# Optimization experiments

Hardware: AMD Instinct MI355X
Metric: run time of the kernel (lower is better)

Reference implementation:

```python
import jax, jax.numpy as jnp
import numpy as np

DN = ('NCHW', 'OIHW', 'NCHW')

def bn(x, g, b, m, v, eps=1e-5):
    # inference-mode BatchNorm2d over channel dim of NCHW
    s = g * jax.lax.rsqrt(v + eps)
    return x * s[:, None, None] + (b - m * s)[:, None, None]

def conv2d(x, w, pad):
    return jax.lax.conv_general_dilated(x, w, (1, 1), pad, dimension_numbers=DN)

def mamba(x, in_w, cw, cb, xp_w, dt_w, dt_b, A_log, Dp, out_w):
    # x: [B, L, d_model]
    B, L, dm = x.shape
    di = cw.shape[0]           # d_inner
    N = A_log.shape[1]         # d_state
    R = dt_w.shape[1]          # dt_rank
    K = cw.shape[2]            # d_conv
    xz = x @ in_w.T            # [B, L, 2*di]
    xi, z = xz[..., :di], xz[..., di:]
    # causal depthwise conv1d along L
    xc = jnp.transpose(xi, (0, 2, 1))  # [B, di, L]
    xc = jax.lax.conv_general_dilated(xc, cw, (1,), [(K - 1, 0)],
                                      dimension_numbers=('NCH', 'OIH', 'NCH'),
                                      feature_group_count=di)
    xc = jax.nn.silu(xc + cb[None, :, None])
    xc = jnp.transpose(xc, (0, 2, 1))  # [B, L, di]
    dbl = xc @ xp_w.T                  # [B, L, R+2N]
    dt, Bs, Cs = dbl[..., :R], dbl[..., R:R + N], dbl[..., R + N:]
    dt = jax.nn.softplus(dt @ dt_w.T + dt_b)        # [B, L, di]
    A = -jnp.exp(A_log)                              # [di, N]
    dA = jnp.exp(dt[..., None] * A)                  # [B, L, di, N]
    dBx = dt[..., None] * Bs[:, :, None, :] * xc[..., None]  # [B, L, di, N]

    def step(h, inp):
        a, bx, c = inp                               # [B,di,N],[B,di,N],[B,N]
        h = a * h + bx
        return h, jnp.einsum('bdn,bn->bd', h, c)

    h0 = jnp.zeros((B, di, N), x.dtype)
    _, ys = jax.lax.scan(step, h0, (jnp.transpose(dA, (1, 0, 2, 3)),
                                    jnp.transpose(dBx, (1, 0, 2, 3)),
                                    jnp.transpose(Cs, (1, 0, 2))))
    y = jnp.transpose(ys, (1, 0, 2)) + xc * Dp       # skip via D
    y = y * jax.nn.silu(z)                           # gate
    return y @ out_w.T                               # [B, L, dm]

def fwd(x, w1, g1, b1, m1, v1, w2, g2, b2, m2, v2,
        in_w, cw, cb, xp_w, dt_w, dt_b, A_log, Dp, out_w,
        w3, g3, b3, m3, v3, w4, g4, b4, m4, v4):
    x = jax.nn.gelu(bn(conv2d(x, w1, [(1, 1), (1, 1)]), g1, b1, m1, v1), approximate=False)
    x = jax.nn.silu(bn(conv2d(x, w2, [(0, 0), (0, 0)]), g2, b2, m2, v2))
    Bsz, Dc, H, W = x.shape
    t = jnp.transpose(x, (0, 2, 3, 1)).reshape(Bsz, H * W, Dc)
    t = mamba(t, in_w, cw, cb, xp_w, dt_w, dt_b, A_log, Dp, out_w)
    x = jnp.transpose(t.reshape(Bsz, H, W, Dc), (0, 3, 1, 2))
    x = jax.nn.silu(bn(conv2d(x, w3, [(0, 0), (0, 0)]), g3, b3, m3, v3))
    x = jax.nn.gelu(bn(conv2d(x, w4, [(1, 1), (1, 1)]), g4, b4, m4, v4), approximate=False)
    return x

def setup_inputs() -> dict:
    INC, D, OUTC = 96, 192, 192
    DI, N, R, K = 2 * D, 16, 12, 4   # d_inner, d_state, dt_rank, d_conv
    B, H, W = 8, 32, 32
    ks = jax.random.split(jax.random.key(0), 32)
    rn = lambda i, sh, s=0.05: s * jax.random.normal(ks[i], sh, dtype=jnp.float32)
    def bnp(i, c):
        k1, k2, k3, k4 = jax.random.split(ks[i], 4)
        return (1.0 + 0.1 * jax.random.normal(k1, (c,), dtype=jnp.float32),
                0.1 * jax.random.normal(k2, (c,), dtype=jnp.float32),
                0.1 * jax.random.normal(k3, (c,), dtype=jnp.float32),
                jax.random.uniform(k4, (c,), jnp.float32, 0.5, 1.5))
    g1, b1, m1, v1 = bnp(2, INC)
    g2, b2, m2, v2 = bnp(4, D)
    g3, b3, m3, v3 = bnp(6, OUTC)
    g4, b4, m4, v4 = bnp(8, OUTC)
    A_log = jnp.log(jnp.broadcast_to(jnp.arange(1, N + 1, dtype=jnp.float32), (DI, N)))
    return {
        'x': jax.random.normal(ks[0], (B, INC, H, W), dtype=jnp.float32),
        'w1': rn(1, (INC, INC, 3, 3)), 'g1': g1, 'b1': b1, 'm1': m1, 'v1': v1,
        'w2': rn(3, (D, INC, 1, 1)), 'g2': g2, 'b2': b2, 'm2': m2, 'v2': v2,
        'in_w': rn(10, (2 * DI, D), 0.02),
        'cw': rn(11, (DI, 1, K), 0.2),
        'cb': rn(12, (DI,), 0.02),
        'xp_w': rn(13, (R + 2 * N, DI), 0.05),
        'dt_w': rn(14, (DI, R), 0.1),
        'dt_b': rn(15, (DI,), 0.1) - 4.0,
        'A_log': A_log,
        'Dp': jnp.ones((DI,), dtype=jnp.float32),
        'out_w': rn(16, (D, DI), 0.05),
        'w3': rn(5, (OUTC, D, 1, 1)), 'g3': g3, 'b3': b3, 'm3': m3, 'v3': v3,
        'w4': rn(7, (OUTC, OUTC, 3, 3), 0.03), 'g4': g4, 'b4': b4, 'm4': m4, 'v4': v4,
    }

def reference(x, w1, g1, b1, m1, v1, w2, g2, b2, m2, v2,
              in_w, cw, cb, xp_w, dt_w, dt_b, A_log, Dp, out_w,
              w3, g3, b3, m3, v3, w4, g4, b4, m4, v4):
    return fwd(x, w1, g1, b1, m1, v1, w2, g2, b2, m2, v2,
               in_w, cw, cb, xp_w, dt_w, dt_b, A_log, Dp, out_w,
               w3, g3, b3, m3, v3, w4, g4, b4, m4, v4)
```

## Files before the change

kernel.cpp:

```cpp
#include <hip/hip_runtime.h>
#include <hip/hip_bf16.h>

using u16 = unsigned short;
using short8 = __attribute__((ext_vector_type(8))) short;
using f32x4  = __attribute__((ext_vector_type(4))) float;

constexpr int DI_ = 384;

constexpr size_t O_XZ   = 0;
constexpr size_t O_XCT  = O_XZ  + (size_t)8192*384;
constexpr size_t O_ZST  = O_XCT + (size_t)384*8192;
constexpr size_t O_DBLT = O_ZST + (size_t)384*8192;
constexpr size_t O_YFT  = O_DBLT+ (size_t)32*8192;
constexpr size_t O_B16  = O_YFT + (size_t)384*8192;
constexpr size_t O_DTT  = O_XZ;
constexpr size_t B_T1  = 0;
constexpr size_t B_T2  = B_T1  + (size_t)8192*96;
constexpr size_t B_XC  = B_T2  + (size_t)8192*192;
constexpr size_t B_XB1 = B_XC  + (size_t)8192*384;
constexpr size_t B_XB4 = B_XB1 + (size_t)8192*96;
constexpr size_t B_WT1 = B_XB4 + (size_t)8192*192;
constexpr size_t B_WT4 = B_WT1 + (size_t)9*96*96;
constexpr size_t B_INW = B_WT4 + (size_t)9*192*192;
constexpr size_t B_W2  = B_INW + (size_t)768*192;
constexpr size_t B_XP  = B_W2  + (size_t)192*96;
constexpr size_t B_WDT = B_XP  + (size_t)32*384;
constexpr size_t B_WOW = B_WDT + (size_t)384*384;

__device__ __forceinline__ u16 f2b(float f) {
    __hip_bfloat16 h = __float2bfloat16(f);
    return *reinterpret_cast<u16*>(&h);
}

struct PrepArgs {
    const float *w1, *w4, *in_w, *w2, *xp_w, *dt_w, *w3, *out_w, *x;
    u16 *wt1, *wt4, *inwb, *w2b, *xpb, *Wdt, *Wow, *Xb1;
};

__global__ __launch_bounds__(256) void prep_k(PrepArgs a) {
    const int job = blockIdx.y;
    const int stride = gridDim.x * 256;
    const int i0 = blockIdx.x * 256 + threadIdx.x;
    switch (job) {
    case 0:
        for (int i = i0; i < 9*96*96; i += stride) {
            int ci = i % 96, co = (i / 96) % 96, t = i / (96*96);
            a.wt1[i] = f2b(a.w1[((size_t)co*96 + ci)*9 + t]);
        } break;
    case 1:
        for (int i = i0; i < 9*192*192; i += stride) {
            int ci = i % 192, co = (i / 192) % 192, t = i / (192*192);
            a.wt4[i] = f2b(a.w4[((size_t)co*192 + ci)*9 + t]);
        } break;
    case 2:
        for (int i = i0; i < 768*192; i += stride) a.inwb[i] = f2b(a.in_w[i]);
        break;
    case 3:
        for (int i = i0; i < 192*96; i += stride) a.w2b[i] = f2b(a.w2[i]);
        break;
    case 4:
        for (int i = i0; i < 32*384; i += stride) {
            int r = i / 384, c = i % 384;
            a.xpb[i] = f2b(a.xp_w[(size_t)(12 + r)*384 + c]);
        } break;
    case 5:
        for (int i = i0; i < 384*384; i += stride) {
            int r = i / 384, c = i % 384;
            float s = 0.f;
            #pragma unroll
            for (int k = 0; k < 12; ++k) s += a.dt_w[r*12 + k] * a.xp_w[(size_t)k*384 + c];
            a.Wdt[i] = f2b(s);
        } break;
    case 6:
        for (int i = i0; i < 192*384; i += stride) {
            int o = i / 384, d = i % 384;
            float s = 0.f;
            for (int j = 0; j < 192; ++j) s += a.w3[(size_t)o*192 + j] * a.out_w[(size_t)j*384 + d];
            a.Wow[i] = f2b(s);
        } break;
    case 7:
        for (int i = i0; i < 8192*96; i += stride) {
            int ci = i % 96, px = i / 96;
            a.Xb1[i] = f2b(a.x[(((size_t)(px >> 10) * 96 + ci) << 10) | (size_t)(px & 1023)]);
        } break;
    }
}

template<int CIN, int COUT, int NTILE, int OUTM>
__global__ __launch_bounds__(256) void conv3x3_mfma_k(
    const u16* __restrict__ Xb, const u16* __restrict__ Wt,
    const float* __restrict__ g, const float* __restrict__ b,
    const float* __restrict__ m, const float* __restrict__ v,
    void* __restrict__ out)
{
    constexpr int LDA = 40;
    constexpr int NT = NTILE / 16;
    __shared__ u16 As[64 * LDA];
    __shared__ u16 Bs[NTILE * LDA];
    const int tid = threadIdx.x;
    const int wave = tid >> 6, lane = tid & 63;
    const int quad = lane >> 4, l16 = lane & 15;
    const int rowBase = blockIdx.x * 64;
    const int colBase = blockIdx.y * NTILE;

    f32x4 acc[NT];
    #pragma unroll
    for (int nt = 0; nt < NT; ++nt)
        #pragma unroll
        for (int i = 0; i < 4; ++i) acc[nt][i] = 0.f;

    const int ar = tid >> 2, aseg = tid & 3;
    const int apx = rowBase + ar;
    const int ah = (apx >> 5) & 31, aw = apx & 31;

    for (int t = 0; t < 9; ++t) {
        const int dr = t / 3 - 1, dc = t % 3 - 1;
        const bool avalid = ((unsigned)(ah + dr) < 32u) && ((unsigned)(aw + dc) < 32u);
        const int apxs = apx + dr * 32 + dc;
        for (int ci0 = 0; ci0 < CIN; ci0 += 32) {
            __syncthreads();
            uint4 va = make_uint4(0u, 0u, 0u, 0u);
            if (avalid)
                va = *(const uint4*)(Xb + (size_t)apxs * CIN + ci0 + aseg * 8);
            *(uint4*)(As + ar * LDA + aseg * 8) = va;
            if (tid < NTILE * 4) {
                int r = tid >> 2, seg = tid & 3;
                uint4 vb = *(const uint4*)(Wt + ((size_t)t * COUT + colBase + r) * CIN + ci0 + seg * 8);
                *(uint4*)(Bs + r * LDA + seg * 8) = vb;
            }
            __syncthreads();
            short8 a = *(const short8*)(As + (wave * 16 + l16) * LDA + quad * 8);
            #pragma unroll
            for (int nt = 0; nt < NT; ++nt) {
                short8 bf = *(const short8*)(Bs + (nt * 16 + l16) * LDA + quad * 8);
                acc[nt] = __builtin_amdgcn_mfma_f32_16x16x32_bf16(a, bf, acc[nt], 0, 0, 0);
            }
        }
    }

    const int px0 = rowBase + wave * 16 + quad * 4;
    #pragma unroll
    for (int nt = 0; nt < NT; ++nt) {
        const int co = colBase + nt * 16 + l16;
        const float sc = g[co] * rsqrtf(v[co] + 1e-5f);
        const float bb = b[co] - m[co] * sc;
        float o[4];
        #pragma unroll
        for (int r = 0; r < 4; ++r) {
            float xv = acc[nt][r] * sc + bb;
            o[r] = 0.5f * xv * (1.f + erff(xv * 0.70710678f));
        }
        if (OUTM == 2) {
            #pragma unroll
            for (int r = 0; r < 4; ++r)
                ((u16*)out)[(size_t)(px0 + r) * COUT + co] = f2b(o[r]);
        } else {
            const int img = px0 >> 10, off = px0 & 1023;
            *(float4*)((float*)out + (((size_t)img * COUT + co) << 10) + off) =
                make_float4(o[0], o[1], o[2], o[3]);
        }
    }
}

template<int NTILE, int EPI, int OUTM>
__device__ __forceinline__ void gemm_body(
    int M, int N, int K,
    const u16* __restrict__ Ab, const u16* __restrict__ Bb, void* __restrict__ C,
    const float* __restrict__ p0, const float* __restrict__ p1,
    const float* __restrict__ p2, const float* __restrict__ p3,
    int rowBase, int colBase, u16* As, u16* Bs)
{
    constexpr int LDA = 40;
    constexpr int NT = NTILE / 16;
    const int tid = threadIdx.x;
    const int wave = tid >> 6, lane = tid & 63;
    const int quad = lane >> 4, l16 = lane & 15;

    f32x4 acc[NT];
    #pragma unroll
    for (int nt = 0; nt < NT; ++nt)
        #pragma unroll
        for (int i = 0; i < 4; ++i) acc[nt][i] = 0.f;

    const int ar = tid >> 2, aseg = tid & 3;

    for (int k0 = 0; k0 < K; k0 += 32) {
        __syncthreads();
        uint4 va = *(const uint4*)(Ab + (size_t)(rowBase + ar) * K + k0 + aseg * 8);
        *(uint4*)(As + ar * LDA + aseg * 8) = va;
        if (tid < NTILE * 4) {
            int r = tid >> 2, seg = tid & 3;
            uint4 vb = *(const uint4*)(Bb + (size_t)(colBase + r) * K + k0 + seg * 8);
            *(uint4*)(Bs + r * LDA + seg * 8) = vb;
        }
        __syncthreads();
        short8 a = *(const short8*)(As + (wave * 16 + l16) * LDA + quad * 8);
        #pragma unroll
        for (int nt = 0; nt < NT; ++nt) {
            short8 bf = *(const short8*)(Bs + (nt * 16 + l16) * LDA + quad * 8);
            acc[nt] = __builtin_amdgcn_mfma_f32_16x16x32_bf16(a, bf, acc[nt], 0, 0, 0);
        }
    }

    const int px0 = rowBase + wave * 16 + quad * 4;
    #pragma unroll
    for (int nt = 0; nt < NT; ++nt) {
        const int co = colBase + nt * 16 + l16;
        float sc = 0.f, bb = 0.f;
        if (EPI == 1) {
            sc = p0[co] * rsqrtf(p3[co] + 1e-5f);
            bb = p1[co] - p2[co] * sc;
        } else if (EPI == 2) {
            bb = p0[co];
        }
        float o[4];
        #pragma unroll
        for (int r = 0; r < 4; ++r) {
            float xv = acc[nt][r];
            if (EPI == 1) {
                xv = xv * sc + bb;
                xv = xv / (1.f + __expf(-xv));
            } else if (EPI == 2) {
                xv += bb;
                xv = (xv > 20.f) ? xv : log1pf(__expf(xv));
            } else if (EPI == 3) {
                xv = xv / (1.f + __expf(-xv));
            }
            o[r] = xv;
        }
        if (OUTM == 3) {
            *(float4*)((float*)C + (size_t)co * M + px0) =
                make_float4(o[0], o[1], o[2], o[3]);
        } else if (OUTM == 2) {
            #pragma unroll
            for (int r = 0; r < 4; ++r)
                ((u16*)C)[(size_t)(px0 + r) * N + co] = f2b(o[r]);
        } else {
            #pragma unroll
            for (int r = 0; r < 4; ++r)
                ((float*)C)[(size_t)(px0 + r) * N + co] = o[r];
        }
    }
}

template<int NTILE, int EPI, int OUTM>
__global__ __launch_bounds__(256) void gemm_mfma_k(
    int M, int N, int K,
    const u16* __restrict__ Ab, const u16* __restrict__ Bb, void* __restrict__ C,
    const float* __restrict__ p0, const float* __restrict__ p1,
    const float* __restrict__ p2, const float* __restrict__ p3)
{
    __shared__ u16 As[64 * 40];
    __shared__ u16 Bs[NTILE * 40];
    gemm_body<NTILE, EPI, OUTM>(M, N, K, Ab, Bb, C, p0, p1, p2, p3,
                                blockIdx.x * 64, blockIdx.y * NTILE, As, Bs);
}

__global__ __launch_bounds__(256) void pd_k(
    const u16* __restrict__ xcb, const u16* __restrict__ Wdt,
    const u16* __restrict__ xpb, const float* __restrict__ dt_b,
    float* __restrict__ dtt, float* __restrict__ dblt)
{
    __shared__ u16 As[64 * 40];
    __shared__ u16 Bs[64 * 40];
    if (blockIdx.y < 6) {
        gemm_body<64, 2, 3>(8192, 384, 384, xcb, Wdt, dtt, dt_b, nullptr, nullptr, nullptr,
                            blockIdx.x * 64, blockIdx.y * 64, As, Bs);
    } else {
        gemm_body<32, 0, 3>(8192, 32, 384, xcb, xpb, dblt, nullptr, nullptr, nullptr, nullptr,
                            blockIdx.x * 64, 0, As, Bs);
    }
}

__global__ __launch_bounds__(256) void gemm_at_k(
    int M, int N, int K,
    const float* __restrict__ At, const u16* __restrict__ Bb, u16* __restrict__ C,
    const float* __restrict__ p0, const float* __restrict__ p1,
    const float* __restrict__ p2, const float* __restrict__ p3)
{
    constexpr int LDA = 40;
    constexpr int NTILE = 64, NT = 4;
    __shared__ u16 As[64 * LDA];
    __shared__ u16 Bs[NTILE * LDA];
    const int tid = threadIdx.x;
    const int wave = tid >> 6, lane = tid & 63;
    const int quad = lane >> 4, l16 = lane & 15;
    const int rowBase = blockIdx.x * 64;
    const int colBase = blockIdx.y * NTILE;

    f32x4 acc[NT];
    #pragma unroll
    for (int nt = 0; nt < NT; ++nt)
        #pragma unroll
        for (int i = 0; i < 4; ++i) acc[nt][i] = 0.f;

    const int krow = tid >> 3, mseg = tid & 7;

    for (int k0 = 0; k0 < K; k0 += 32) {
        __syncthreads();
        const float* src = At + (size_t)(k0 + krow) * M + rowBase + mseg * 4;
        float4 f0 = *(const float4*)(src);
        float4 f1 = *(const float4*)(src + 32);
        As[(mseg*4 + 0) * LDA + krow] = f2b(f0.x);
        As[(mseg*4 + 1) * LDA + krow] = f2b(f0.y);
        As[(mseg*4 + 2) * LDA + krow] = f2b(f0.z);
        As[(mseg*4 + 3) * LDA + krow] = f2b(f0.w);
        As[(mseg*4 + 32) * LDA + krow] = f2b(f1.x);
        As[(mseg*4 + 33) * LDA + krow] = f2b(f1.y);
        As[(mseg*4 + 34) * LDA + krow] = f2b(f1.z);
        As[(mseg*4 + 35) * LDA + krow] = f2b(f1.w);
        if (tid < NTILE * 4) {
            int r = tid >> 2, seg = tid & 3;
            uint4 vb = *(const uint4*)(Bb + (size_t)(colBase + r) * K + k0 + seg * 8);
            *(uint4*)(Bs + r * LDA + seg * 8) = vb;
        }
        __syncthreads();
        short8 a = *(const short8*)(As + (wave * 16 + l16) * LDA + quad * 8);
        #pragma unroll
        for (int nt = 0; nt < NT; ++nt) {
            short8 bf = *(const short8*)(Bs + (nt * 16 + l16) * LDA + quad * 8);
            acc[nt] = __builtin_amdgcn_mfma_f32_16x16x32_bf16(a, bf, acc[nt], 0, 0, 0);
        }
    }

    const int px0 = rowBase + wave * 16 + quad * 4;
    #pragma unroll
    for (int nt = 0; nt < NT; ++nt) {
        const int co = colBase + nt * 16 + l16;
        const float sc = p0[co] * rsqrtf(p3[co] + 1e-5f);
        const float bb = p1[co] - p2[co] * sc;
        #pragma unroll
        for (int r = 0; r < 4; ++r) {
            float xv = acc[nt][r] * sc + bb;
            xv = xv / (1.f + __expf(-xv));
            C[(size_t)(px0 + r) * N + co] = f2b(xv);
        }
    }
}

__global__ __launch_bounds__(256) void dwconv_k(
    const float* __restrict__ xz, const float* __restrict__ cw, const float* __restrict__ cb,
    u16* __restrict__ xcb, float* __restrict__ xct)
{
    __shared__ float T[64][65];
    const int tid = threadIdx.x;
    const int cl = tid & 63, rq = tid >> 6;
    const int mBase = blockIdx.x * 64, cBase = blockIdx.y * 64;
    const int c = cBase + cl;
    const float w0 = cw[c*4+0], w1 = cw[c*4+1], w2 = cw[c*4+2], w3 = cw[c*4+3];
    const float bias = cb[c];
    #pragma unroll
    for (int rr = 0; rr < 16; ++rr) {
        int ml = rr * 4 + rq;
        int bl = mBase + ml;
        int l = bl & 1023;
        float acc = bias + xz[(size_t)bl * 384 + c] * w3;
        if (l >= 1) acc += xz[(size_t)(bl-1) * 384 + c] * w2;
        if (l >= 2) acc += xz[(size_t)(bl-2) * 384 + c] * w1;
        if (l >= 3) acc += xz[(size_t)(bl-3) * 384 + c] * w0;
        float s = acc / (1.f + __expf(-acc));
        xcb[(size_t)bl * DI_ + c] = f2b(s);
        T[ml][cl] = s;
    }
    __syncthreads();
    #pragma unroll
    for (int rr = 0; rr < 16; ++rr) {
        int dl = rr * 4 + rq;
        xct[(size_t)(cBase + dl) * 8192 + mBase + cl] = T[cl][dl];
    }
}

__global__ __launch_bounds__(256) void scan_k(
    const float* __restrict__ dtt, const float* __restrict__ dblt,
    const float* __restrict__ xct, const float* __restrict__ zst,
    const float* __restrict__ A_log, const float* __restrict__ Dp,
    float* __restrict__ yft)
{
    const int bd = blockIdx.x;
    const int b = bd / DI_, d = bd % DI_;
    const int tid = threadIdx.x;
    const size_t tb = (size_t)d * 8192 + (size_t)b * 1024;
    const size_t nb = (size_t)b * 1024;
    const int t4 = tid * 4;

    __shared__ float LH[16][257];
    __shared__ float SD[257];
    __shared__ float SH[16][17];
    __shared__ float SP[16][17];
    __shared__ float SSD[17];
    __shared__ float AndS[16];

    const float4 dt4 = *(const float4*)(dtt + tb + t4);
    const float4 xc4 = *(const float4*)(xct + tb + t4);
    const float dtxc[4] = {dt4.x*xc4.x, dt4.y*xc4.y, dt4.z*xc4.z, dt4.w*xc4.w};

    float And[16];
    #pragma unroll
    for (int n = 0; n < 16; ++n) And[n] = -__expf(A_log[d*16 + n]);
    if (tid < 16) AndS[tid] = -__expf(A_log[d*16 + tid]);
    SD[tid] = dt4.x + dt4.y + dt4.z + dt4.w;

    #pragma unroll
    for (int n = 0; n < 16; ++n) {
        const float4 bs4 = *(const float4*)(dblt + (size_t)n * 8192 + nb + t4);
        float h = dtxc[0] * bs4.x;
        h = __expf(dt4.y * And[n]) * h + dtxc[1] * bs4.y;
        h = __expf(dt4.z * And[n]) * h + dtxc[2] * bs4.z;
        h = __expf(dt4.w * And[n]) * h + dtxc[3] * bs4.w;
        LH[n][tid] = h;
    }
    __syncthreads();

    {
        const int n = tid & 15, s = tid >> 4;
        const float An = AndS[n];
        float H = 0.f, ssd = 0.f;
        #pragma unroll
        for (int k = 0; k < 16; ++k) {
            const int c = s * 16 + k;
            float sd = SD[c];
            H = __expf(An * sd) * H + LH[n][c];
            ssd += sd;
        }
        SH[n][s] = H;
        if (n == 0) SSD[s] = ssd;
    }
    __syncthreads();

    if (tid < 16) {
        const float An = AndS[tid];
        float Hp = 0.f;
        #pragma unroll
        for (int s = 0; s < 16; ++s) {
            SP[tid][s] = Hp;
            Hp = __expf(An * SSD[s]) * Hp + SH[tid][s];
        }
    }
    __syncthreads();

    {
        const int n = tid & 15, s = tid >> 4;
        const float An = AndS[n];
        float st = SP[n][s];
        #pragma unroll
        for (int k = 0; k < 16; ++k) {
            const int c = s * 16 + k;
            float a = __expf(An * SD[c]);
            float h = LH[n][c];
            LH[n][c] = st;
            st = a * st + h;
        }
    }
    __syncthreads();

    float y0 = 0.f, y1 = 0.f, y2 = 0.f, y3 = 0.f;
    #pragma unroll
    for (int n = 0; n < 16; ++n) {
        float h = LH[n][tid];
        const float4 bs4 = *(const float4*)(dblt + (size_t)n * 8192 + nb + t4);
        const float4 cs4 = *(const float4*)(dblt + (size_t)(16 + n) * 8192 + nb + t4);
        h = __expf(dt4.x * And[n]) * h + dtxc[0]*bs4.x; y0 += h * cs4.x;
        h = __expf(dt4.y * And[n]) * h + dtxc[1]*bs4.y; y1 += h * cs4.y;
        h = __expf(dt4.z * And[n]) * h + dtxc[2]*bs4.z; y2 += h * cs4.z;
        h = __expf(dt4.w * And[n]) * h + dtxc[3]*bs4.w; y3 += h * cs4.w;
    }
    const float dp = Dp[d];
    const float4 zs4 = *(const float4*)(zst + tb + t4);
    float4 o;
    o.x = (y0 + xc4.x * dp) * zs4.x;
    o.y = (y1 + xc4.y * dp) * zs4.y;
    o.z = (y2 + xc4.z * dp) * zs4.z;
    o.w = (y3 + xc4.w * dp) * zs4.w;
    *(float4*)(yft + tb + t4) = o;
}

extern "C" void kernel_launch(void* const* d_in, const int* in_sizes, int n_in,
                              void* d_out, int out_size, void* d_ws, size_t ws_size,
                              hipStream_t stream) {
    const float* x     = (const float*)d_in[0];
    const float* w1    = (const float*)d_in[1];
    const float* g1    = (const float*)d_in[2];
    const float* b1    = (const float*)d_in[3];
    const float* m1    = (const float*)d_in[4];
    const float* v1    = (const float*)d_in[5];
    const float* w2    = (const float*)d_in[6];
    const float* g2    = (const float*)d_in[7];
    const float* b2    = (const float*)d_in[8];
    const float* m2    = (const float*)d_in[9];
    const float* v2    = (const float*)d_in[10];
    const float* in_w  = (const float*)d_in[11];
    const float* cw    = (const float*)d_in[12];
    const float* cb    = (const float*)d_in[13];
    const float* xp_w  = (const float*)d_in[14];
    const float* dt_w  = (const float*)d_in[15];
    const float* dt_b  = (const float*)d_in[16];
    const float* A_log = (const float*)d_in[17];
    const float* Dp    = (const float*)d_in[18];
    const float* out_w = (const float*)d_in[19];
    const float* w3    = (const float*)d_in[20];
    const float* g3    = (const float*)d_in[21];
    const float* b3    = (const float*)d_in[22];
    const float* m3    = (const float*)d_in[23];
    const float* v3    = (const float*)d_in[24];
    const float* w4    = (const float*)d_in[25];
    const float* g4    = (const float*)d_in[26];
    const float* b4    = (const float*)d_in[27];
    const float* m4    = (const float*)d_in[28];
    const float* v4    = (const float*)d_in[29];

    float* ws   = (float*)d_ws;
    float* xzb  = ws + O_XZ;
    float* xct  = ws + O_XCT;
    float* zst  = ws + O_ZST;
    float* dblt = ws + O_DBLT;
    float* yft  = ws + O_YFT;
    float* dtt  = ws + O_DTT;
    u16* b16  = (u16*)(ws + O_B16);
    u16* t1b  = b16 + B_T1;
    u16* t2b  = b16 + B_T2;
    u16* xcb  = b16 + B_XC;
    u16* Xb1  = b16 + B_XB1;
    u16* Xb4  = b16 + B_XB4;
    u16* wt1  = b16 + B_WT1;
    u16* wt4  = b16 + B_WT4;
    u16* inwb = b16 + B_INW;
    u16* w2b  = b16 + B_W2;
    u16* xpb  = b16 + B_XP;
    u16* Wdt  = b16 + B_WDT;
    u16* Wow  = b16 + B_WOW;

    PrepArgs pa;
    pa.w1 = w1; pa.w4 = w4; pa.in_w = in_w; pa.w2 = w2; pa.xp_w = xp_w;
    pa.dt_w = dt_w; pa.w3 = w3; pa.out_w = out_w; pa.x = x;
    pa.wt1 = wt1; pa.wt4 = wt4; pa.inwb = inwb; pa.w2b = w2b; pa.xpb = xpb;
    pa.Wdt = Wdt; pa.Wow = Wow; pa.Xb1 = Xb1;
    prep_k<<<dim3(256, 8), 256, 0, stream>>>(pa);

    conv3x3_mfma_k<96, 96, 32, 2><<<dim3(128, 3), 256, 0, stream>>>(
        Xb1, wt1, g1, b1, m1, v1, t1b);

    gemm_mfma_k<64, 1, 2><<<dim3(128, 3), 256, 0, stream>>>(
        8192, 192, 96, t1b, w2b, t2b, g2, b2, m2, v2);

    gemm_mfma_k<64, 0, 0><<<dim3(128, 6), 256, 0, stream>>>(
        8192, 384, 192, t2b, inwb, xzb, nullptr, nullptr, nullptr, nullptr);

    gemm_mfma_k<64, 3, 3><<<dim3(128, 6), 256, 0, stream>>>(
        8192, 384, 192, t2b, inwb + (size_t)384*192, zst, nullptr, nullptr, nullptr, nullptr);

    dwconv_k<<<dim3(128, 6), 256, 0, stream>>>(xzb, cw, cb, xcb, xct);

    pd_k<<<dim3(128, 7), 256, 0, stream>>>(xcb, Wdt, xpb, dt_b, dtt, dblt);

    scan_k<<<8 * DI_, 256, 0, stream>>>(dtt, dblt, xct, zst, A_log, Dp, yft);

    gemm_at_k<<<dim3(128, 3), 256, 0, stream>>>(
        8192, 192, 384, yft, Wow, Xb4, g3, b3, m3, v3);

    conv3x3_mfma_k<192, 192, 64, 1><<<dim3(128, 3), 256, 0, stream>>>(
        Xb4, wt4, g4, b4, m4, v4, (float*)d_out);
}
```

Baseline: 277.2 us.

## Stage conv3x3 input halo tile once per channel chunk and merge in_proj GEMMs

The 3x3 convolution kernel now loads a 4x34 halo of input pixels into shared memory once per 32-channel chunk, along with the weights for all nine taps. All nine tap MFMAs then run from that staged data, which cuts the global reloads and barriers that came with iterating over taps in the outer loop. The cost is a much larger shared-memory footprint, mainly the 9*NTILE weight buffer, which may lower occupancy. Separately, the two in_proj GEMM launches are merged into one kernel with a 12-column grid, saving one launch.

```diff
diff --git a/kernel.cpp b/kernel.cpp
--- a/kernel.cpp
+++ b/kernel.cpp
@@ -93,15 +93,25 @@
     const float* __restrict__ m, const float* __restrict__ v,
     void* __restrict__ out)
 {
-    constexpr int LDA = 40;
+    constexpr int LD = 40;
     constexpr int NT = NTILE / 16;
-    __shared__ u16 As[64 * LDA];
-    __shared__ u16 Bs[NTILE * LDA];
+    __shared__ u16 As[4 * 36 * LD];
+    __shared__ u16 Bs[9 * NTILE * LD];
     const int tid = threadIdx.x;
     const int wave = tid >> 6, lane = tid & 63;
     const int quad = lane >> 4, l16 = lane & 15;
     const int rowBase = blockIdx.x * 64;
     const int colBase = blockIdx.y * NTILE;
+    const int img = rowBase >> 10;
+    const int imgRow0 = (rowBase & 1023) >> 5;
+
+    if (tid < 160) {
+        int slot8 = tid / 20;
+        int off = tid % 20;
+        int hrow = slot8 >> 1;
+        int hcol = (slot8 & 1) ? 33 : 0;
+        ((unsigned*)As)[((hrow * 36 + hcol) * LD) / 2 + off] = 0u;
+    }
 
     f32x4 acc[NT];
     #pragma unroll
@@ -109,30 +119,41 @@
         #pragma unroll
         for (int i = 0; i < 4; ++i) acc[nt][i] = 0.f;
 
-    const int ar = tid >> 2, aseg = tid & 3;
-    const int apx = rowBase + ar;
-    const int ah = (apx >> 5) & 31, aw = apx & 31;
-
-    for (int t = 0; t < 9; ++t) {
-        const int dr = t / 3 - 1, dc = t % 3 - 1;
-        const bool avalid = ((unsigned)(ah + dr) < 32u) && ((unsigned)(aw + dc) < 32u);
-        const int apxs = apx + dr * 32 + dc;
-        for (int ci0 = 0; ci0 < CIN; ci0 += 32) {
-            __syncthreads();
+    const int pxl = wave * 16 + l16;
+    const int prow = pxl >> 5, pcol = pxl & 31;
+
+    for (int ci0 = 0; ci0 < CIN; ci0 += 32) {
+        __syncthreads();
+        #pragma unroll
+        for (int it = 0; it < 2; ++it) {
+            int id = tid + it * 256;
+            int pix = id >> 2, seg = id & 3;
+            int hrow = pix >> 5, hcol = pix & 31;
+            int grow = imgRow0 - 1 + hrow;
             uint4 va = make_uint4(0u, 0u, 0u, 0u);
-            if (avalid)
-                va = *(const uint4*)(Xb + (size_t)apxs * CIN + ci0 + aseg * 8);
-            *(uint4*)(As + ar * LDA + aseg * 8) = va;
-            if (tid < NTILE * 4) {
-                int r = tid >> 2, seg = tid & 3;
-                uint4 vb = *(const uint4*)(Wt + ((size_t)t * COUT + colBase + r) * CIN + ci0 + seg * 8);
-                *(uint4*)(Bs + r * LDA + seg * 8) = vb;
-            }
-            __syncthreads();
-            short8 a = *(const short8*)(As + (wave * 16 + l16) * LDA + quad * 8);
+            if ((unsigned)grow < 32u)
+                va = *(const uint4*)(Xb +
+                    (size_t)((img << 10) + (grow << 5) + hcol) * CIN + ci0 + seg * 8);
+            *(uint4*)(As + (hrow * 36 + hcol + 1) * LD + seg * 8) = va;
+        }
+        constexpr int BT = 9 * NTILE * 4;
+        for (int id = tid; id < BT; id += 256) {
+            int t = id / (NTILE * 4);
+            int r = (id >> 2) & (NTILE - 1);
+            int seg = id & 3;
+            uint4 vb = *(const uint4*)(Wt +
+                ((size_t)t * COUT + colBase + r) * CIN + ci0 + seg * 8);
+            *(uint4*)(Bs + (t * NTILE + r) * LD + seg * 8) = vb;
+        }
+        __syncthreads();
+        #pragma unroll
+        for (int t = 0; t < 9; ++t) {
+            const int dr = t / 3 - 1, dc = t % 3 - 1;
+            short8 a = *(const short8*)(As +
+                ((prow + 1 + dr) * 36 + (pcol + 1 + dc)) * LD + quad * 8);
             #pragma unroll
             for (int nt = 0; nt < NT; ++nt) {
-                short8 bf = *(const short8*)(Bs + (nt * 16 + l16) * LDA + quad * 8);
+                short8 bf = *(const short8*)(Bs + (t * NTILE + nt * 16 + l16) * LD + quad * 8);
                 acc[nt] = __builtin_amdgcn_mfma_f32_16x16x32_bf16(a, bf, acc[nt], 0, 0, 0);
             }
         }
@@ -155,8 +176,8 @@
             for (int r = 0; r < 4; ++r)
                 ((u16*)out)[(size_t)(px0 + r) * COUT + co] = f2b(o[r]);
         } else {
-            const int img = px0 >> 10, off = px0 & 1023;
-            *(float4*)((float*)out + (((size_t)img * COUT + co) << 10) + off) =
+            const int oimg = px0 >> 10, off = px0 & 1023;
+            *(float4*)((float*)out + (((size_t)oimg * COUT + co) << 10) + off) =
                 make_float4(o[0], o[1], o[2], o[3]);
         }
     }
@@ -254,6 +275,23 @@
     __shared__ u16 Bs[NTILE * 40];
     gemm_body<NTILE, EPI, OUTM>(M, N, K, Ab, Bb, C, p0, p1, p2, p3,
                                 blockIdx.x * 64, blockIdx.y * NTILE, As, Bs);
+}
+
+__global__ __launch_bounds__(256) void ip_k(
+    const u16* __restrict__ t2b, const u16* __restrict__ inwb,
+    float* __restrict__ xzb, float* __restrict__ zst)
+{
+    __shared__ u16 As[64 * 40];
+    __shared__ u16 Bs[64 * 40];
+    if (blockIdx.y < 6) {
+        gemm_body<64, 0, 0>(8192, 384, 192, t2b, inwb, xzb,
+                            nullptr, nullptr, nullptr, nullptr,
+                            blockIdx.x * 64, blockIdx.y * 64, As, Bs);
+    } else {
+        gemm_body<64, 3, 3>(8192, 384, 192, t2b, inwb + (size_t)384*192, zst,
+                            nullptr, nullptr, nullptr, nullptr,
+                            blockIdx.x * 64, (blockIdx.y - 6) * 64, As, Bs);
+    }
 }
 
 __global__ __launch_bounds__(256) void pd_k(
@@ -542,11 +580,7 @@
     gemm_mfma_k<64, 1, 2><<<dim3(128, 3), 256, 0, stream>>>(
         8192, 192, 96, t1b, w2b, t2b, g2, b2, m2, v2);
 
-    gemm_mfma_k<64, 0, 0><<<dim3(128, 6), 256, 0, stream>>>(
-        8192, 384, 192, t2b, inwb, xzb, nullptr, nullptr, nullptr, nullptr);
-
-    gemm_mfma_k<64, 3, 3><<<dim3(128, 6), 256, 0, stream>>>(
-        8192, 384, 192, t2b, inwb + (size_t)384*192, zst, nullptr, nullptr, nullptr, nullptr);
+    ip_k<<<dim3(128, 12), 256, 0, stream>>>(t2b, inwb, xzb, zst);
 
     dwconv_k<<<dim3(128, 6), 256, 0, stream>>>(xzb, cw, cb, xcb, xct);
 
```

After: 264.7 us. 4.5% less time.
